# Optimization experiments

Measured on AMD Instinct MI355X. Metric: run time of the kernel, lower is better.

## Reference

```python
import jax, jax.numpy as jnp
import numpy as np

D_IN, D, SEQ, B = 512, 1024, 2048, 8
EPS = 1e-5


def positional_encoding(seq_len, d):
    pos = np.arange(seq_len)[:, None].astype(np.float32)
    i = np.arange(d)[None, :].astype(np.float32)
    angle_rads = pos / (10000.0 ** (2.0 * np.floor(i / 2.0) / np.float32(d)))
    angle_rads[:, 0::2] = np.sin(angle_rads[:, 0::2])
    angle_rads[:, 1::2] = np.cos(angle_rads[:, 1::2])
    return jnp.asarray(angle_rads[None, ...], dtype=jnp.float32)  # [1, s, d]


def setup_inputs() -> dict:
    key = jax.random.key(0)
    ks = jax.random.split(key, 10)
    def lin(k, fan_in, shape):
        bound = 1.0 / np.sqrt(fan_in)
        return jax.random.uniform(k, shape, jnp.float32, -bound, bound)
    return {
        "inputs": jax.random.normal(ks[0], (B, SEQ, D_IN), jnp.float32),
        "embed_w": lin(ks[1], D_IN, (D, D_IN)),
        "embed_b": lin(ks[2], D_IN, (D,)),
        "wq_w": lin(ks[3], D, (D, D)), "wq_b": lin(ks[3], D, (D,)),
        "wk_w": lin(ks[4], D, (D, D)), "wk_b": lin(ks[4], D, (D,)),
        "wv_w": lin(ks[5], D, (D, D)), "wv_b": lin(ks[5], D, (D,)),
        "ln_g": jnp.ones((D,), jnp.float32),
        "ln_b": jnp.zeros((D,), jnp.float32),
        "soft_key_w": lin(ks[6], D, (D, D)),
        "soft_query": jax.random.normal(ks[7], (D,), jnp.float32),
        "pos_enc": positional_encoding(SEQ, D),
    }


def reference(inputs, embed_w, embed_b, wq_w, wq_b, wk_w, wk_b, wv_w, wv_b,
              ln_g, ln_b, soft_key_w, soft_query, pos_enc):
    x = jnp.einsum('bsi,oi->bso', inputs, embed_w) + embed_b  # embed
    x = x + pos_enc  # broadcast positional encoding over batch
    Q = jnp.einsum('bsd,od->bso', x, wq_w) + wq_b
    K = jnp.einsum('bsd,od->bso', x, wk_w) + wk_b
    V = jnp.einsum('bsd,od->bso', x, wv_w) + wv_b
    score = jnp.einsum('bso,bio->bsi', Q, K) / jnp.sqrt(jnp.float32(D))
    score = jax.nn.softmax(score, axis=2)
    Z = jnp.einsum('bsi,bio->bso', score, V)
    h = x + Z
    mu = jnp.mean(h, axis=-1, keepdims=True)
    var = jnp.mean(jnp.square(h - mu), axis=-1, keepdims=True)
    H = (h - mu) * jax.lax.rsqrt(var + EPS) * ln_g + ln_b
    soft_key = jnp.tanh(jnp.einsum('bsd,od->bso', H, soft_key_w))
    soft_score = jax.nn.softmax(jnp.einsum('bso,o->bs', soft_key, soft_query), axis=1)
    return jnp.einsum('bs,bso->bo', soft_score, H)
```

## Files before the change

### kernel.cpp

```cpp
#include <hip/hip_runtime.h>
#include <hip/hip_bf16.h>
#include <math.h>

typedef __bf16 bf16_t;
typedef bf16_t bf16x8 __attribute__((ext_vector_type(8)));
typedef bf16_t bf16x4 __attribute__((ext_vector_type(4)));
typedef float  f32x4  __attribute__((ext_vector_type(4)));

#define D_IN   512
#define DMODEL 1024
#define SEQ    2048
#define BATCH  8
#define NTOK   (BATCH*SEQ)

typedef __attribute__((address_space(1))) unsigned int gu32;
typedef __attribute__((address_space(3))) unsigned int lu32;

__device__ __forceinline__ void async16(const void* g, void* l) {
    __builtin_amdgcn_global_load_lds((gu32*)g, (lu32*)l, 16, 0, 0);
}

template<int EPI>
__global__ __launch_bounds__(256)
void gemm_bt(const bf16_t* __restrict__ Ab, const bf16_t* __restrict__ Bb,
             bf16_t* __restrict__ Cb, int K, int ldc, int gx, int gy,
             long batchA, long batchB, long batchC,
             const float* __restrict__ bias, const float* __restrict__ aux_f,
             const bf16_t* __restrict__ resid, float* __restrict__ logits,
             const float* __restrict__ bias3)
{
    __shared__ __align__(16) bf16_t smem[32768];

    const int tid  = threadIdx.x;
    const int lane = tid & 63;
    const int wave = tid >> 6;

    const int flat = blockIdx.x;
    const int nb   = gridDim.x;
    const int vid  = (flat & 7) * (nb >> 3) + (flat >> 3);
    const int pb   = gx * gy;
    const int z    = vid / pb;
    const int w    = vid - z * pb;
    const int sy   = w / (gx * 4);
    const int r    = w - sy * (gx * 4);
    const int sx   = r >> 4;
    const int inner= r & 15;
    const int mtile = (sy * 4 + (inner & 3)) * 128;
    const int ntile = (sx * 4 + (inner >> 2)) * 128;

    const bf16_t* A  = Ab + (long)z * batchA;
    const bf16_t* Bp = Bb + (long)z * batchB;

    f32x4 acc[4][4];
    #pragma unroll
    for (int i = 0; i < 4; ++i)
        #pragma unroll
        for (int j = 0; j < 4; ++j)
            acc[i][j] = (f32x4)(0.f);

    const int lr  = lane & 15;
    const int lr7 = lr & 7;
    const int lq  = lane >> 4;

    const int wrow = (wave >> 1) * 64;
    const int wcol = (wave & 1) * 64;

    const int srow8 = lane >> 3;
    const int sk    = ((lane & 7) ^ srow8) * 8;

    {
        bf16_t* Ad = smem;
        bf16_t* Bd = smem + 8192;
        #pragma unroll
        for (int j = 0; j < 4; ++j) {
            const int g   = (wave << 2) + j;
            const int row = (g << 3) + srow8;
            async16(A  + (long)(mtile + row) * K + sk, &Ad[g << 9]);
            async16(Bp + (long)(ntile + row) * K + sk, &Bd[g << 9]);
        }
    }

    int cur = 0;
    for (int k0 = 0; k0 < K; k0 += 64) {
        __syncthreads();
        if (k0 + 64 < K) {
            bf16_t* Ad = smem + ((cur ^ 1) << 14);
            bf16_t* Bd = Ad + 8192;
            const int kn = k0 + 64;
            #pragma unroll
            for (int j = 0; j < 4; ++j) {
                const int g   = (wave << 2) + j;
                const int row = (g << 3) + srow8;
                async16(A  + (long)(mtile + row) * K + (kn + sk), &Ad[g << 9]);
                async16(Bp + (long)(ntile + row) * K + (kn + sk), &Bd[g << 9]);
            }
        }
        const bf16_t* Ar = smem + (cur << 14);
        const bf16_t* Br = Ar + 8192;
        #pragma unroll
        for (int s = 0; s < 2; ++s) {
            const int po = ((lq + (s << 2)) ^ lr7) << 3;
            bf16x8 af[4], bf[4];
            #pragma unroll
            for (int t = 0; t < 4; ++t)
                af[t] = *(const bf16x8*)&Ar[(wrow + t*16 + lr)*64 + po];
            #pragma unroll
            for (int t = 0; t < 4; ++t)
                bf[t] = *(const bf16x8*)&Br[(wcol + t*16 + lr)*64 + po];
            #pragma unroll
            for (int tr = 0; tr < 4; ++tr)
                #pragma unroll
                for (int tc = 0; tc < 4; ++tc)
                    acc[tr][tc] = __builtin_amdgcn_mfma_f32_16x16x32_bf16(
                                      af[tr], bf[tc], acc[tr][tc], 0, 0, 0);
        }
        cur ^= 1;
    }

    if constexpr (EPI == 5) {
        const int mbase = mtile + wrow + lq*4;
        #pragma unroll
        for (int tr = 0; tr < 4; ++tr) {
            #pragma unroll
            for (int reg = 0; reg < 4; ++reg) {
                const int m = mbase + tr*16 + reg;
                float rs = 0.f;
                #pragma unroll
                for (int tc = 0; tc < 4; ++tc) {
                    const int n = ntile + wcol + tc*16 + lr;
                    rs += tanhf(acc[tr][tc][reg]) * aux_f[n];
                }
                rs += __shfl_xor(rs, 1);
                rs += __shfl_xor(rs, 2);
                rs += __shfl_xor(rs, 4);
                rs += __shfl_xor(rs, 8);
                if (lr == 0) atomicAdd(&logits[m], rs);
            }
        }
        return;
    }

    __syncthreads();

    if constexpr (EPI == 4) {
        float* fsm = (float*)smem;
        #pragma unroll
        for (int tr = 0; tr < 4; ++tr) {
            #pragma unroll
            for (int reg = 0; reg < 4; ++reg) {
                const int rl = wrow + tr*16 + lq*4 + reg;
                #pragma unroll
                for (int tc = 0; tc < 4; ++tc) {
                    const int cl = wcol + tc*16 + lr;
                    fsm[rl*128 + ((((cl >> 2) ^ (rl & 31)) << 2) | (cl & 3))] = acc[tr][tc][reg];
                }
            }
        }
        __syncthreads();
        bf16_t* C = Cb + (long)z * batchC;
        const float* rsum = bias + (long)z * SEQ;
        const int chunk = tid & 15;
        const int grp   = tid >> 4;
        #pragma unroll
        for (int rep = 0; rep < 8; ++rep) {
            const int R  = grp + rep*16;
            const int c0 = chunk*8;
            const int p0 = (((c0 >> 2)       ^ (R & 31)) << 2);
            const int p1 = ((((c0 + 4) >> 2) ^ (R & 31)) << 2);
            const f32x4 f0 = *(const f32x4*)&fsm[R*128 + p0];
            const f32x4 f1 = *(const f32x4*)&fsm[R*128 + p1];
            const float inv = 1.f / rsum[mtile + R];
            const long off = (long)(mtile + R)*ldc + ntile + c0;
            const bf16x8 r8 = *(const bf16x8*)&resid[(long)z*batchC + off];
            bf16x8 val;
            #pragma unroll
            for (int i = 0; i < 4; ++i) {
                val[i]     = (bf16_t)(f0[i]*inv + (float)r8[i]);
                val[i + 4] = (bf16_t)(f1[i]*inv + (float)r8[i + 4]);
            }
            *(bf16x8*)&C[off] = val;
        }
        return;
    }

    const int seg = (EPI == 6) ? (ntile >> 10) : 0;
    const float* bp = bias;
    if constexpr (EPI == 6) bp = (seg == 0) ? bias : (seg == 1) ? aux_f : bias3;

    #pragma unroll
    for (int tr = 0; tr < 4; ++tr) {
        #pragma unroll
        for (int reg = 0; reg < 4; ++reg) {
            const int rl = wrow + tr*16 + lq*4 + reg;
            #pragma unroll
            for (int tc = 0; tc < 4; ++tc) {
                const int cl = wcol + tc*16 + lr;
                float v = acc[tr][tc][reg];
                if constexpr (EPI == 0)
                    v += bias[ntile + cl] + aux_f[((mtile + rl) & (SEQ-1))*DMODEL + ntile + cl];
                if constexpr (EPI == 3) v = __expf(v * 0.03125f);
                if constexpr (EPI == 6) v += bp[(ntile + cl) & 1023];
                smem[rl*128 + ((((cl >> 3) ^ (rl & 7)) << 3) | (cl & 7))] = (bf16_t)v;
            }
        }
    }
    __syncthreads();

    if constexpr (EPI == 3) {
        bf16_t* C = Cb + (long)z * batchC;
        float* rsum = logits + (long)z * SEQ;
        const int chunk = tid & 15;
        const int grp   = tid >> 4;
        #pragma unroll
        for (int rep = 0; rep < 8; ++rep) {
            const int R = grp + rep*16;
            const int phys = chunk ^ (R & 7);
            bf16x8 val = *(const bf16x8*)&smem[R*128 + phys*8];
            const long off = (long)(mtile + R)*ldc + ntile + chunk*8;
            *(bf16x8*)&C[off] = val;
            float ps = 0.f;
            #pragma unroll
            for (int i = 0; i < 8; ++i) ps += (float)val[i];
            ps += __shfl_xor(ps, 1);
            ps += __shfl_xor(ps, 2);
            ps += __shfl_xor(ps, 4);
            ps += __shfl_xor(ps, 8);
            if (chunk == 0) atomicAdd(&rsum[mtile + R], ps);
        }
        return;
    }

    if constexpr (EPI == 6) {
        if (seg == 2) {
            bf16_t* VTb = Cb + 33554432;
            const int col  = tid & 127;
            const int half = tid >> 7;
            const int b    = mtile >> 11, s0 = mtile & (SEQ-1);
            const long nbase = (long)b*DMODEL + (ntile & 1023) + col;
            #pragma unroll
            for (int rep = 0; rep < 8; ++rep) {
                const int R0 = half*64 + rep*8;
                bf16x8 o;
                #pragma unroll
                for (int i = 0; i < 8; ++i) {
                    const int rl = R0 + i;
                    o[i] = smem[rl*128 + ((((col >> 3) ^ (rl & 7)) << 3) | (col & 7))];
                }
                *(bf16x8*)&VTb[nbase*SEQ + s0 + R0] = o;
            }
            return;
        }
        const int chunk = tid & 15;
        const int grp   = tid >> 4;
        const long base = (long)seg * 16777216 + (ntile & 1023) + chunk*8;
        #pragma unroll
        for (int rep = 0; rep < 8; ++rep) {
            const int R = grp + rep*16;
            const int phys = chunk ^ (R & 7);
            bf16x8 val = *(const bf16x8*)&smem[R*128 + phys*8];
            *(bf16x8*)&Cb[base + (long)(mtile + R)*1024] = val;
        }
        return;
    }

    bf16_t* C = Cb + (long)z * batchC;
    const int chunk = tid & 15;
    const int grp   = tid >> 4;
    #pragma unroll
    for (int rep = 0; rep < 8; ++rep) {
        const int R = grp + rep*16;
        const int phys = chunk ^ (R & 7);
        bf16x8 val = *(const bf16x8*)&smem[R*128 + phys*8];
        const long off = (long)(mtile + R)*ldc + ntile + chunk*8;
        *(bf16x8*)&C[off] = val;
    }
}

__global__ __launch_bounds__(256) void cast_all(
        const float* __restrict__ inp, const float* __restrict__ emw,
        const float* __restrict__ wqw, const float* __restrict__ wkw,
        const float* __restrict__ wvw, const float* __restrict__ skw,
        bf16_t* __restrict__ in_b, bf16_t* __restrict__ we_b,
        bf16_t* __restrict__ wq_b, bf16_t* __restrict__ wk_b,
        bf16_t* __restrict__ wv_b, bf16_t* __restrict__ sk_b,
        float* __restrict__ logits, float* __restrict__ rowsum) {
    const int i = blockIdx.x*256 + threadIdx.x;
    const float* s; bf16_t* d; int j;
    if      (i < 2097152) { s = inp; d = in_b; j = i; }
    else if (i < 2228224) { s = emw; d = we_b; j = i - 2097152; }
    else if (i < 2490368) { s = wqw; d = wq_b; j = i - 2228224; }
    else if (i < 2752512) { s = wkw; d = wk_b; j = i - 2490368; }
    else if (i < 3014656) { s = wvw; d = wv_b; j = i - 2752512; }
    else if (i < 3276800) { s = skw; d = sk_b; j = i - 3014656; }
    else if (i < 3280896) { ((f32x4*)logits)[i - 3276800] = (f32x4)(0.f); return; }
    else                  { ((f32x4*)rowsum)[i - 3280896] = (f32x4)(0.f); return; }
    const float4 f = ((const float4*)s)[j];
    bf16x4 o;
    o[0] = (bf16_t)f.x; o[1] = (bf16_t)f.y; o[2] = (bf16_t)f.z; o[3] = (bf16_t)f.w;
    ((bf16x4*)d)[j] = o;
}

__global__ __launch_bounds__(256) void layernorm_k(const bf16_t* __restrict__ h, bf16_t* __restrict__ H,
                                                   const float* __restrict__ gam, const float* __restrict__ bet) {
    const long row = blockIdx.x;
    const bf16_t* hr = h + row*DMODEL;
    bf16_t* Hr = H + row*DMODEL;
    const int t = threadIdx.x, lane = t & 63, wave = t >> 6;
    __shared__ float sm[8];
    const bf16x4 hv = *(const bf16x4*)&hr[t*4];
    float v[4]; float s = 0.f, q = 0.f;
    #pragma unroll
    for (int j = 0; j < 4; ++j) { v[j] = (float)hv[j]; s += v[j]; q += v[j]*v[j]; }
    #pragma unroll
    for (int o = 32; o; o >>= 1) { s += __shfl_xor(s, o); q += __shfl_xor(q, o); }
    if (lane == 0) { sm[wave] = s; sm[4 + wave] = q; }
    __syncthreads();
    s = (sm[0] + sm[1]) + (sm[2] + sm[3]);
    q = (sm[4] + sm[5]) + (sm[6] + sm[7]);
    const float mu  = s * (1.f/DMODEL);
    const float var = q * (1.f/DMODEL) - mu*mu;
    const float r   = rsqrtf(var + 1e-5f);
    const float4 g4 = ((const float4*)gam)[t];
    const float4 b4 = ((const float4*)bet)[t];
    bf16x4 o4;
    o4[0] = (bf16_t)((v[0] - mu)*r*g4.x + b4.x);
    o4[1] = (bf16_t)((v[1] - mu)*r*g4.y + b4.y);
    o4[2] = (bf16_t)((v[2] - mu)*r*g4.z + b4.z);
    o4[3] = (bf16_t)((v[3] - mu)*r*g4.w + b4.w);
    *(bf16x4*)&Hr[t*4] = o4;
}

__global__ __launch_bounds__(256) void pool_partial(const float* __restrict__ logits,
                                                    const bf16_t* __restrict__ H,
                                                    float* __restrict__ part) {
    const int b = blockIdx.y;
    const int c = blockIdx.x;
    const int t = threadIdx.x, lane = t & 63, wave = t >> 6;
    __shared__ float sm[8];
    __shared__ float wsm[32];
    const float* lb = logits + b*SEQ;
    const float4 a4 = ((const float4*)lb)[t];
    const float4 c4 = ((const float4*)lb)[t + 256];
    float v[8] = {a4.x, a4.y, a4.z, a4.w, c4.x, c4.y, c4.z, c4.w};
    float mx = -3.0e38f;
    #pragma unroll
    for (int j = 0; j < 8; ++j) mx = fmaxf(mx, v[j]);
    #pragma unroll
    for (int o = 32; o; o >>= 1) mx = fmaxf(mx, __shfl_xor(mx, o));
    if (lane == 0) sm[wave] = mx;
    __syncthreads();
    mx = fmaxf(fmaxf(sm[0], sm[1]), fmaxf(sm[2], sm[3]));
    float s = 0.f;
    #pragma unroll
    for (int j = 0; j < 8; ++j) s += __expf(v[j] - mx);
    #pragma unroll
    for (int o = 32; o; o >>= 1) s += __shfl_xor(s, o);
    if (lane == 0) sm[4 + wave] = s;
    __syncthreads();
    s = (sm[4] + sm[5]) + (sm[6] + sm[7]);
    const float inv = 1.f / s;
    if (t < 32) wsm[t] = __expf(lb[c*32 + t] - mx) * inv;
    __syncthreads();

    const bf16_t* Hb = H + ((long)b*SEQ + (long)c*32)*DMODEL;
    f32x4 acc = (f32x4)(0.f);
    #pragma unroll 4
    for (int i = 0; i < 32; ++i) {
        const float wi = wsm[i];
        const bf16x4 hv = *(const bf16x4*)&Hb[(long)i*DMODEL + t*4];
        acc[0] += wi * (float)hv[0];
        acc[1] += wi * (float)hv[1];
        acc[2] += wi * (float)hv[2];
        acc[3] += wi * (float)hv[3];
    }
    *(f32x4*)&part[((long)b*64 + c)*DMODEL + t*4] = acc;
}

__global__ __launch_bounds__(256) void pool_reduce(const float* __restrict__ part,
                                                   float* __restrict__ out) {
    const int i = blockIdx.x*256 + threadIdx.x;
    const int b = i >> 10, o = i & 1023;
    const float* p = part + (long)b*64*DMODEL + o;
    float s = 0.f;
    #pragma unroll
    for (int c = 0; c < 64; ++c) s += p[c*DMODEL];
    out[i] = s;
}

extern "C" void kernel_launch(void* const* d_in, const int* in_sizes, int n_in,
                              void* d_out, int out_size, void* d_ws, size_t ws_size,
                              hipStream_t stream) {
    (void)in_sizes; (void)n_in; (void)out_size; (void)ws_size;
    const float* inp = (const float*)d_in[0];
    const float* emw = (const float*)d_in[1];
    const float* emb = (const float*)d_in[2];
    const float* wqw = (const float*)d_in[3];
    const float* wqb = (const float*)d_in[4];
    const float* wkw = (const float*)d_in[5];
    const float* wkb = (const float*)d_in[6];
    const float* wvw = (const float*)d_in[7];
    const float* wvb = (const float*)d_in[8];
    const float* lng = (const float*)d_in[9];
    const float* lnb = (const float*)d_in[10];
    const float* skw = (const float*)d_in[11];
    const float* sq  = (const float*)d_in[12];
    const float* pos = (const float*)d_in[13];
    float* out = (float*)d_out;

    char* ws = (char*)d_ws;
    bf16_t* in_b   = (bf16_t*)(ws + 0);
    bf16_t* we_b   = (bf16_t*)(ws + 16777216);
    bf16_t* wq_b   = (bf16_t*)(ws + 17825792);
    bf16_t* wk_b   = (bf16_t*)(ws + 19922944);
    bf16_t* wv_b   = (bf16_t*)(ws + 22020096);
    bf16_t* sk_b   = (bf16_t*)(ws + 24117248);
    float*  logits = (float*)(ws + 26214400);
    float*  rowsum = (float*)(ws + 26279936);
    bf16_t* xb     = (bf16_t*)(ws + 26345472);
    bf16_t* Qb     = (bf16_t*)(ws + 59899904);
    bf16_t* Kb     = (bf16_t*)(ws + 93454336);
    bf16_t* VT     = (bf16_t*)(ws + 127008768);
    bf16_t* Hb     = (bf16_t*)(ws + 160563200);
    bf16_t* Pb     = (bf16_t*)(ws + 194117632);
    float*  part   = (float*)(ws + 0);

    cast_all<<<12832, 256, 0, stream>>>(inp, emw, wqw, wkw, wvw, skw,
                                        in_b, we_b, wq_b, wk_b, wv_b, sk_b,
                                        logits, rowsum);

    gemm_bt<0><<<1024, 256, 0, stream>>>(in_b, we_b, xb, D_IN, DMODEL, 8, 128,
        0, 0, 0, emb, pos, nullptr, nullptr, nullptr);
    gemm_bt<6><<<3072, 256, 0, stream>>>(xb, wq_b, Qb, DMODEL, DMODEL, 24, 128,
        0, 0, 0, wqb, wkb, nullptr, nullptr, wvb);
    gemm_bt<3><<<2048, 256, 0, stream>>>(Qb, Kb, Pb, DMODEL, SEQ, 16, 16,
        (long)SEQ*DMODEL, (long)SEQ*DMODEL, (long)SEQ*SEQ, nullptr, nullptr, nullptr, rowsum, nullptr);
    gemm_bt<4><<<1024, 256, 0, stream>>>(Pb, VT, Qb, SEQ, DMODEL, 8, 16,
        (long)SEQ*SEQ, (long)DMODEL*SEQ, (long)SEQ*DMODEL, rowsum, nullptr, xb, nullptr, nullptr);
    layernorm_k<<<NTOK, 256, 0, stream>>>(Qb, Hb, lng, lnb);
    gemm_bt<5><<<1024, 256, 0, stream>>>(Hb, sk_b, nullptr, DMODEL, 0, 8, 128,
        0, 0, 0, nullptr, sq, nullptr, logits, nullptr);
    pool_partial<<<dim3(64, BATCH), 256, 0, stream>>>(logits, Hb, part);
    pool_reduce<<<32, 256, 0, stream>>>(part, out);
}
```

Before: 490.9 us.

## Enlarge GEMM tiles to 256x256 with 8 waves and phased LDS pipeline

Reworks the shared GEMM kernel from 128x128 tiles with 4 waves to 256x256 tiles with 8 waves (512 threads). The main loop becomes an 8-phase schedule that interleaves LDS fragment reads, async global-to-LDS prefetch of quarter tiles, and MFMA bursts, using explicit barriers, vmcnt waits and setprio. All epilogues are adapted to the larger tile, and EPI 4 stages its output in two halves to fit LDS. The aim is more operand reuse per loaded byte and better overlap of memory with compute. The costs are more registers and LDS per block and fewer blocks per launch.

```diff
diff --git a/kernel.cpp b/kernel.cpp
--- a/kernel.cpp
+++ b/kernel.cpp
@@ -20,8 +20,58 @@
     __builtin_amdgcn_global_load_lds((gu32*)g, (lu32*)l, 16, 0, 0);
 }
 
+
+#define PH_DS(AB_, BB_, QM, QN)                                               \
+    _Pragma("unroll")                                                         \
+    for (int s_ = 0; s_ < 2; ++s_) {                                          \
+        const int po_ = (((s_ << 2) | lq) ^ lr7) << 3;                        \
+        _Pragma("unroll")                                                     \
+        for (int t_ = 0; t_ < 4; ++t_)                                        \
+            af[s_][t_] = *(const bf16x8*)&(AB_)[(wrow + (QM)*64 + t_*16 + lr)*64 + po_]; \
+        _Pragma("unroll")                                                     \
+        for (int u_ = 0; u_ < 2; ++u_)                                        \
+            bfv[s_][u_] = *(const bf16x8*)&(BB_)[(wcol + (QN)*32 + u_*16 + lr)*64 + po_]; \
+    }
+
+#define PH_MM(QM, QN)                                                         \
+    __builtin_amdgcn_s_barrier();                                             \
+    asm volatile("s_waitcnt lgkmcnt(0)");                                     \
+    __builtin_amdgcn_s_setprio(1);                                            \
+    _Pragma("unroll")                                                         \
+    for (int s_ = 0; s_ < 2; ++s_) {                                          \
+        _Pragma("unroll")                                                     \
+        for (int t_ = 0; t_ < 4; ++t_) {                                      \
+            _Pragma("unroll")                                                 \
+            for (int u_ = 0; u_ < 2; ++u_)                                    \
+                acc[(QM)*4 + t_][(QN)*2 + u_] =                               \
+                    __builtin_amdgcn_mfma_f32_16x16x32_bf16(af[s_][t_], bfv[s_][u_], \
+                        acc[(QM)*4 + t_][(QN)*2 + u_], 0, 0, 0);              \
+        }                                                                     \
+    }                                                                         \
+    __builtin_amdgcn_s_setprio(0);
+
+#define PH_END                                                                \
+    __builtin_amdgcn_s_barrier();                                             \
+    asm volatile("" ::: "memory");
+
+#define STAGE_A(Q, DST, KO) {                                                 \
+    _Pragma("unroll")                                                         \
+    for (int j_ = 0; j_ < 2; ++j_) {                                          \
+        const int i_ = (wid << 1) | j_;                                       \
+        const int g_ = i_ + (i_ & 8) + ((Q) << 3);                            \
+        async16(Ag + (long)((g_ << 3) + srow8) * K + (KO) + sk, (DST) + (g_ << 9)); \
+    } }
+
+#define STAGE_B(Q, DST, KO) {                                                 \
+    _Pragma("unroll")                                                         \
+    for (int j_ = 0; j_ < 2; ++j_) {                                          \
+        const int i_ = (wid << 1) | j_;                                       \
+        const int g_ = (((i_ & 12) << 1) | (i_ & 3)) + ((Q) << 2);            \
+        async16(Bg + (long)((g_ << 3) + srow8) * K + (KO) + sk, (DST) + (g_ << 9)); \
+    } }
+
 template<int EPI>
-__global__ __launch_bounds__(256)
+__global__ __launch_bounds__(512, 2)
 void gemm_bt(const bf16_t* __restrict__ Ab, const bf16_t* __restrict__ Bb,
              bf16_t* __restrict__ Cb, int K, int ldc, int gx, int gy,
              long batchA, long batchB, long batchC,
@@ -29,11 +79,13 @@
              const bf16_t* __restrict__ resid, float* __restrict__ logits,
              const float* __restrict__ bias3)
 {
-    __shared__ __align__(16) bf16_t smem[32768];
+    __shared__ __align__(16) bf16_t smem[65536];
 
     const int tid  = threadIdx.x;
     const int lane = tid & 63;
-    const int wave = tid >> 6;
+    const int wid  = tid >> 6;
+    const int wr   = wid >> 2;
+    const int wc   = wid & 3;
 
     const int flat = blockIdx.x;
     const int nb   = gridDim.x;
@@ -45,15 +97,15 @@
     const int r    = w - sy * (gx * 4);
     const int sx   = r >> 4;
     const int inner= r & 15;
-    const int mtile = (sy * 4 + (inner & 3)) * 128;
-    const int ntile = (sx * 4 + (inner >> 2)) * 128;
-
-    const bf16_t* A  = Ab + (long)z * batchA;
-    const bf16_t* Bp = Bb + (long)z * batchB;
-
-    f32x4 acc[4][4];
-    #pragma unroll
-    for (int i = 0; i < 4; ++i)
+    const int mtile = (sy * 4 + (inner & 3)) * 256;
+    const int ntile = (sx * 4 + (inner >> 2)) * 256;
+
+    const bf16_t* Ag = Ab + (long)z * batchA + (long)mtile * K;
+    const bf16_t* Bg = Bb + (long)z * batchB + (long)ntile * K;
+
+    f32x4 acc[8][4];
+    #pragma unroll
+    for (int i = 0; i < 8; ++i)
         #pragma unroll
         for (int j = 0; j < 4; ++j)
             acc[i][j] = (f32x4)(0.f);
@@ -61,74 +113,84 @@
     const int lr  = lane & 15;
     const int lr7 = lr & 7;
     const int lq  = lane >> 4;
-
-    const int wrow = (wave >> 1) * 64;
-    const int wcol = (wave & 1) * 64;
+    const int wrow = wr * 128;
+    const int wcol = wc * 64;
 
     const int srow8 = lane >> 3;
     const int sk    = ((lane & 7) ^ srow8) * 8;
 
-    {
-        bf16_t* Ad = smem;
-        bf16_t* Bd = smem + 8192;
+    bf16_t* const A0 = smem;
+    bf16_t* const B0 = smem + 16384;
+    bf16_t* const A1 = smem + 32768;
+    bf16_t* const B1 = smem + 49152;
+
+    const int niter = K >> 7;
+
+    STAGE_A(0, A0, 0);  STAGE_A(1, A0, 0);
+    STAGE_B(0, B0, 0);  STAGE_B(1, B0, 0);
+    STAGE_A(0, A1, 64); STAGE_A(1, A1, 64);
+    STAGE_B(0, B1, 64); STAGE_B(1, B1, 64);
+    asm volatile("s_waitcnt vmcnt(8)" ::: "memory");
+    __builtin_amdgcn_s_barrier();
+    asm volatile("" ::: "memory");
+
+    for (int it = 0; it < niter; ++it) {
+        const int kb = it << 7;
+        const bool nf   = (it > 0);
+        const bool more = (it + 1 < niter);
+        bf16x8 af[2][4], bfv[2][2];
+
+        PH_DS(A0, B0, 0, 0);
+        if (nf) { STAGE_A(1, A1, kb + 64); }
+        PH_MM(0, 0); PH_END;
+
+        PH_DS(A0, B0, 0, 1);
+        if (nf) { STAGE_B(1, B1, kb + 64); }
+        PH_MM(0, 1); PH_END;
+
+        PH_DS(A0, B0, 1, 0);
+        if (more) { STAGE_A(0, A0, kb + 128); }
+        PH_MM(1, 0); PH_END;
+
+        PH_DS(A0, B0, 1, 1);
+        if (more) { STAGE_B(0, B0, kb + 128); }
+        PH_MM(1, 1);
+        if (more) asm volatile("s_waitcnt vmcnt(4)" ::: "memory");
+        else      asm volatile("s_waitcnt vmcnt(0)" ::: "memory");
+        PH_END;
+
+        PH_DS(A1, B1, 0, 0);
+        if (more) { STAGE_A(1, A0, kb + 128); }
+        PH_MM(0, 0); PH_END;
+
+        PH_DS(A1, B1, 0, 1);
+        if (more) { STAGE_B(1, B0, kb + 128); }
+        PH_MM(0, 1); PH_END;
+
+        PH_DS(A1, B1, 1, 0);
+        if (more) { STAGE_A(0, A1, kb + 192); }
+        PH_MM(1, 0); PH_END;
+
+        PH_DS(A1, B1, 1, 1);
+        if (more) { STAGE_B(0, B1, kb + 192); }
+        PH_MM(1, 1);
+        if (more) asm volatile("s_waitcnt vmcnt(4)" ::: "memory");
+        else      asm volatile("s_waitcnt vmcnt(0)" ::: "memory");
+        PH_END;
+    }
+
+    if constexpr (EPI == 5) {
+        const int mb = mtile + wrow + lq * 4;
         #pragma unroll
-        for (int j = 0; j < 4; ++j) {
-            const int g   = (wave << 2) + j;
-            const int row = (g << 3) + srow8;
-            async16(A  + (long)(mtile + row) * K + sk, &Ad[g << 9]);
-            async16(Bp + (long)(ntile + row) * K + sk, &Bd[g << 9]);
-        }
-    }
-
-    int cur = 0;
-    for (int k0 = 0; k0 < K; k0 += 64) {
-        __syncthreads();
-        if (k0 + 64 < K) {
-            bf16_t* Ad = smem + ((cur ^ 1) << 14);
-            bf16_t* Bd = Ad + 8192;
-            const int kn = k0 + 64;
-            #pragma unroll
-            for (int j = 0; j < 4; ++j) {
-                const int g   = (wave << 2) + j;
-                const int row = (g << 3) + srow8;
-                async16(A  + (long)(mtile + row) * K + (kn + sk), &Ad[g << 9]);
-                async16(Bp + (long)(ntile + row) * K + (kn + sk), &Bd[g << 9]);
-            }
-        }
-        const bf16_t* Ar = smem + (cur << 14);
-        const bf16_t* Br = Ar + 8192;
-        #pragma unroll
-        for (int s = 0; s < 2; ++s) {
-            const int po = ((lq + (s << 2)) ^ lr7) << 3;
-            bf16x8 af[4], bf[4];
-            #pragma unroll
-            for (int t = 0; t < 4; ++t)
-                af[t] = *(const bf16x8*)&Ar[(wrow + t*16 + lr)*64 + po];
-            #pragma unroll
-            for (int t = 0; t < 4; ++t)
-                bf[t] = *(const bf16x8*)&Br[(wcol + t*16 + lr)*64 + po];
-            #pragma unroll
-            for (int tr = 0; tr < 4; ++tr)
-                #pragma unroll
-                for (int tc = 0; tc < 4; ++tc)
-                    acc[tr][tc] = __builtin_amdgcn_mfma_f32_16x16x32_bf16(
-                                      af[tr], bf[tc], acc[tr][tc], 0, 0, 0);
-        }
-        cur ^= 1;
-    }
-
-    if constexpr (EPI == 5) {
-        const int mbase = mtile + wrow + lq*4;
-        #pragma unroll
-        for (int tr = 0; tr < 4; ++tr) {
+        for (int fm = 0; fm < 8; ++fm) {
             #pragma unroll
             for (int reg = 0; reg < 4; ++reg) {
-                const int m = mbase + tr*16 + reg;
+                const int m = mb + fm * 16 + reg;
                 float rs = 0.f;
                 #pragma unroll
-                for (int tc = 0; tc < 4; ++tc) {
-                    const int n = ntile + wcol + tc*16 + lr;
-                    rs += tanhf(acc[tr][tc][reg]) * aux_f[n];
+                for (int fn = 0; fn < 4; ++fn) {
+                    const int n = ntile + wcol + fn * 16 + lr;
+                    rs += tanhf(acc[fm][fn][reg]) * aux_f[n];
                 }
                 rs += __shfl_xor(rs, 1);
                 rs += __shfl_xor(rs, 2);
@@ -144,41 +206,48 @@
 
     if constexpr (EPI == 4) {
         float* fsm = (float*)smem;
+        bf16_t* C = Cb + (long)z * batchC;
+        const float* rsum = bias + (long)z * SEQ;
         #pragma unroll
-        for (int tr = 0; tr < 4; ++tr) {
-            #pragma unroll
-            for (int reg = 0; reg < 4; ++reg) {
-                const int rl = wrow + tr*16 + lq*4 + reg;
+        for (int half = 0; half < 2; ++half) {
+            if (half) __syncthreads();
+            if (wr == half) {
                 #pragma unroll
-                for (int tc = 0; tc < 4; ++tc) {
-                    const int cl = wcol + tc*16 + lr;
-                    fsm[rl*128 + ((((cl >> 2) ^ (rl & 31)) << 2) | (cl & 3))] = acc[tr][tc][reg];
+                for (int fm = 0; fm < 8; ++fm) {
+                    #pragma unroll
+                    for (int reg = 0; reg < 4; ++reg) {
+                        const int rl = fm * 16 + lq * 4 + reg;
+                        #pragma unroll
+                        for (int fn = 0; fn < 4; ++fn) {
+                            const int cl = wcol + fn * 16 + lr;
+                            const int ph = (cl >> 2) ^ (rl & 31);
+                            fsm[rl * 256 + (ph << 2) + (cl & 3)] = acc[fm][fn][reg];
+                        }
+                    }
                 }
             }
-        }
-        __syncthreads();
-        bf16_t* C = Cb + (long)z * batchC;
-        const float* rsum = bias + (long)z * SEQ;
-        const int chunk = tid & 15;
-        const int grp   = tid >> 4;
-        #pragma unroll
-        for (int rep = 0; rep < 8; ++rep) {
-            const int R  = grp + rep*16;
-            const int c0 = chunk*8;
-            const int p0 = (((c0 >> 2)       ^ (R & 31)) << 2);
-            const int p1 = ((((c0 + 4) >> 2) ^ (R & 31)) << 2);
-            const f32x4 f0 = *(const f32x4*)&fsm[R*128 + p0];
-            const f32x4 f1 = *(const f32x4*)&fsm[R*128 + p1];
-            const float inv = 1.f / rsum[mtile + R];
-            const long off = (long)(mtile + R)*ldc + ntile + c0;
-            const bf16x8 r8 = *(const bf16x8*)&resid[(long)z*batchC + off];
-            bf16x8 val;
+            __syncthreads();
+            const int chunk = tid & 31;
+            const int grp   = tid >> 5;
             #pragma unroll
-            for (int i = 0; i < 4; ++i) {
-                val[i]     = (bf16_t)(f0[i]*inv + (float)r8[i]);
-                val[i + 4] = (bf16_t)(f1[i]*inv + (float)r8[i + 4]);
+            for (int rep = 0; rep < 8; ++rep) {
+                const int R  = grp + (rep << 4);
+                const int c0 = chunk << 3;
+                const int p0 = (c0 >> 2) ^ (R & 31);
+                const f32x4 f0 = *(const f32x4*)&fsm[R * 256 + (p0 << 2)];
+                const f32x4 f1 = *(const f32x4*)&fsm[R * 256 + ((p0 ^ 1) << 2)];
+                const int Rg = half * 128 + R;
+                const float inv = 1.f / rsum[mtile + Rg];
+                const long off = (long)(mtile + Rg) * ldc + ntile + c0;
+                const bf16x8 r8 = *(const bf16x8*)&resid[(long)z * batchC + off];
+                bf16x8 val;
+                #pragma unroll
+                for (int i = 0; i < 4; ++i) {
+                    val[i]     = (bf16_t)(f0[i] * inv + (float)r8[i]);
+                    val[i + 4] = (bf16_t)(f1[i] * inv + (float)r8[i + 4]);
+                }
+                *(bf16x8*)&C[off] = val;
             }
-            *(bf16x8*)&C[off] = val;
         }
         return;
     }
@@ -188,19 +257,19 @@
     if constexpr (EPI == 6) bp = (seg == 0) ? bias : (seg == 1) ? aux_f : bias3;
 
     #pragma unroll
-    for (int tr = 0; tr < 4; ++tr) {
+    for (int fm = 0; fm < 8; ++fm) {
         #pragma unroll
         for (int reg = 0; reg < 4; ++reg) {
-            const int rl = wrow + tr*16 + lq*4 + reg;
+            const int rl = wrow + fm * 16 + lq * 4 + reg;
             #pragma unroll
-            for (int tc = 0; tc < 4; ++tc) {
-                const int cl = wcol + tc*16 + lr;
-                float v = acc[tr][tc][reg];
+            for (int fn = 0; fn < 4; ++fn) {
+                const int cl = wcol + fn * 16 + lr;
+                float v = acc[fm][fn][reg];
                 if constexpr (EPI == 0)
                     v += bias[ntile + cl] + aux_f[((mtile + rl) & (SEQ-1))*DMODEL + ntile + cl];
                 if constexpr (EPI == 3) v = __expf(v * 0.03125f);
                 if constexpr (EPI == 6) v += bp[(ntile + cl) & 1023];
-                smem[rl*128 + ((((cl >> 3) ^ (rl & 7)) << 3) | (cl & 7))] = (bf16_t)v;
+                smem[rl * 256 + ((((cl >> 3) ^ (rl & 7)) << 3) | (cl & 7))] = (bf16_t)v;
             }
         }
     }
@@ -209,14 +278,14 @@
     if constexpr (EPI == 3) {
         bf16_t* C = Cb + (long)z * batchC;
         float* rsum = logits + (long)z * SEQ;
-        const int chunk = tid & 15;
-        const int grp   = tid >> 4;
+        const int chunk = tid & 31;
+        const int grp   = tid >> 5;
         #pragma unroll
-        for (int rep = 0; rep < 8; ++rep) {
-            const int R = grp + rep*16;
+        for (int rep = 0; rep < 16; ++rep) {
+            const int R = grp + (rep << 4);
             const int phys = chunk ^ (R & 7);
-            bf16x8 val = *(const bf16x8*)&smem[R*128 + phys*8];
-            const long off = (long)(mtile + R)*ldc + ntile + chunk*8;
+            bf16x8 val = *(const bf16x8*)&smem[R * 256 + (phys << 3)];
+            const long off = (long)(mtile + R) * ldc + ntile + (chunk << 3);
             *(bf16x8*)&C[off] = val;
             float ps = 0.f;
             #pragma unroll
@@ -225,6 +294,7 @@
             ps += __shfl_xor(ps, 2);
             ps += __shfl_xor(ps, 4);
             ps += __shfl_xor(ps, 8);
+            ps += __shfl_xor(ps, 16);
             if (chunk == 0) atomicAdd(&rsum[mtile + R], ps);
         }
         return;
@@ -233,45 +303,45 @@
     if constexpr (EPI == 6) {
         if (seg == 2) {
             bf16_t* VTb = Cb + 33554432;
-            const int col  = tid & 127;
-            const int half = tid >> 7;
+            const int col  = tid & 255;
+            const int half = tid >> 8;
             const int b    = mtile >> 11, s0 = mtile & (SEQ-1);
             const long nbase = (long)b*DMODEL + (ntile & 1023) + col;
             #pragma unroll
-            for (int rep = 0; rep < 8; ++rep) {
-                const int R0 = half*64 + rep*8;
+            for (int rep = 0; rep < 16; ++rep) {
+                const int R0 = half * 128 + rep * 8;
                 bf16x8 o;
                 #pragma unroll
                 for (int i = 0; i < 8; ++i) {
                     const int rl = R0 + i;
-                    o[i] = smem[rl*128 + ((((col >> 3) ^ (rl & 7)) << 3) | (col & 7))];
+                    o[i] = smem[rl * 256 + ((((col >> 3) ^ (rl & 7)) << 3) | (col & 7))];
                 }
-                *(bf16x8*)&VTb[nbase*SEQ + s0 + R0] = o;
+                *(bf16x8*)&VTb[nbase * SEQ + s0 + R0] = o;
             }
             return;
         }
-        const int chunk = tid & 15;
-        const int grp   = tid >> 4;
-        const long base = (long)seg * 16777216 + (ntile & 1023) + chunk*8;
+        const int chunk = tid & 31;
+        const int grp   = tid >> 5;
+        const long base = (long)seg * 16777216 + (ntile & 1023) + (chunk << 3);
         #pragma unroll
-        for (int rep = 0; rep < 8; ++rep) {
-            const int R = grp + rep*16;
+        for (int rep = 0; rep < 16; ++rep) {
+            const int R = grp + (rep << 4);
             const int phys = chunk ^ (R & 7);
-            bf16x8 val = *(const bf16x8*)&smem[R*128 + phys*8];
-            *(bf16x8*)&Cb[base + (long)(mtile + R)*1024] = val;
+            bf16x8 val = *(const bf16x8*)&smem[R * 256 + (phys << 3)];
+            *(bf16x8*)&Cb[base + (long)(mtile + R) * 1024] = val;
         }
         return;
     }
 
     bf16_t* C = Cb + (long)z * batchC;
-    const int chunk = tid & 15;
-    const int grp   = tid >> 4;
-    #pragma unroll
-    for (int rep = 0; rep < 8; ++rep) {
-        const int R = grp + rep*16;
+    const int chunk = tid & 31;
+    const int grp   = tid >> 5;
+    #pragma unroll
+    for (int rep = 0; rep < 16; ++rep) {
+        const int R = grp + (rep << 4);
         const int phys = chunk ^ (R & 7);
-        bf16x8 val = *(const bf16x8*)&smem[R*128 + phys*8];
-        const long off = (long)(mtile + R)*ldc + ntile + chunk*8;
+        bf16x8 val = *(const bf16x8*)&smem[R * 256 + (phys << 3)];
+        const long off = (long)(mtile + R) * ldc + ntile + (chunk << 3);
         *(bf16x8*)&C[off] = val;
     }
 }
@@ -428,16 +498,16 @@
                                         in_b, we_b, wq_b, wk_b, wv_b, sk_b,
                                         logits, rowsum);
 
-    gemm_bt<0><<<1024, 256, 0, stream>>>(in_b, we_b, xb, D_IN, DMODEL, 8, 128,
+    gemm_bt<0><<<256, 512, 0, stream>>>(in_b, we_b, xb, D_IN, DMODEL, 4, 64,
         0, 0, 0, emb, pos, nullptr, nullptr, nullptr);
-    gemm_bt<6><<<3072, 256, 0, stream>>>(xb, wq_b, Qb, DMODEL, DMODEL, 24, 128,
+    gemm_bt<6><<<768, 512, 0, stream>>>(xb, wq_b, Qb, DMODEL, DMODEL, 12, 64,
         0, 0, 0, wqb, wkb, nullptr, nullptr, wvb);
-    gemm_bt<3><<<2048, 256, 0, stream>>>(Qb, Kb, Pb, DMODEL, SEQ, 16, 16,
+    gemm_bt<3><<<512, 512, 0, stream>>>(Qb, Kb, Pb, DMODEL, SEQ, 8, 8,
         (long)SEQ*DMODEL, (long)SEQ*DMODEL, (long)SEQ*SEQ, nullptr, nullptr, nullptr, rowsum, nullptr);
-    gemm_bt<4><<<1024, 256, 0, stream>>>(Pb, VT, Qb, SEQ, DMODEL, 8, 16,
+    gemm_bt<4><<<256, 512, 0, stream>>>(Pb, VT, Qb, SEQ, DMODEL, 4, 8,
         (long)SEQ*SEQ, (long)DMODEL*SEQ, (long)SEQ*DMODEL, rowsum, nullptr, xb, nullptr, nullptr);
     layernorm_k<<<NTOK, 256, 0, stream>>>(Qb, Hb, lng, lnb);
-    gemm_bt<5><<<1024, 256, 0, stream>>>(Hb, sk_b, nullptr, DMODEL, 0, 8, 128,
+    gemm_bt<5><<<256, 512, 0, stream>>>(Hb, sk_b, nullptr, DMODEL, 0, 4, 64,
         0, 0, 0, nullptr, sq, nullptr, logits, nullptr);
     pool_partial<<<dim3(64, BATCH), 256, 0, stream>>>(logits, Hb, part);
     pool_reduce<<<32, 256, 0, stream>>>(part, out);
```

After: 502.4 us. 1.02x slower.
